# Performance work log

Hardware: AMD Instinct MI355X
Metric: run time of the kernel (lower is better)

The kernel has to match this reference:

```python
import jax, jax.numpy as jnp
import numpy as np

B, Q, K, H, DQ, DK, DV = 16, 128, 512, 128, 128, 128, 128
MASK_VALUE = -1000000.0  # matches d2l.sequence_mask fill value


def setup_inputs() -> dict:
    key = jax.random.key(0)
    ks = jax.random.split(key, 7)
    queries = jax.random.normal(ks[0], (B, Q, DQ), dtype=jnp.float32)
    keys = jax.random.normal(ks[1], (B, K, DK), dtype=jnp.float32)
    values = jax.random.normal(ks[2], (B, K, DV), dtype=jnp.float32)
    valid_lens = jax.random.randint(ks[3], (B,), 1, K + 1, dtype=jnp.int32)
    # Linear params (no bias), scaled like torch default init ~ 1/sqrt(fan_in)
    W_q = jax.random.normal(ks[4], (DQ, H), dtype=jnp.float32) / np.sqrt(DQ)
    W_k = jax.random.normal(ks[5], (DK, H), dtype=jnp.float32) / np.sqrt(DK)
    w_v = jax.random.normal(ks[6], (H,), dtype=jnp.float32) / np.sqrt(H)
    return {"queries": queries, "keys": keys, "values": values,
            "valid_lens": valid_lens, "W_q": W_q, "W_k": W_k, "w_v": w_v}


def reference(queries, keys, values, valid_lens, W_q, W_k, w_v):
    # Project queries and keys: (B,Q,H), (B,K,H)
    q = jnp.einsum("bqd,dh->bqh", queries, W_q)
    k = jnp.einsum("bkd,dh->bkh", keys, W_k)
    # Broadcast add -> tanh -> linear-to-1 score: (B,Q,K)
    features = jnp.tanh(q[:, :, None, :] + k[:, None, :, :])  # (B,Q,K,H)
    scores = jnp.einsum("bqkh,h->bqk", features, w_v)
    # masked softmax over last axis; valid_lens is (B,), broadcast over Q
    mask = jnp.arange(K)[None, None, :] < valid_lens[:, None, None]  # (B,1,K)
    scores = jnp.where(mask, scores, MASK_VALUE)
    attn = jax.nn.softmax(scores, axis=-1)
    # weighted sum over keys: (B,Q,DV)
    return jnp.einsum("bqk,bkv->bqv", attn, values)
```

## Files before the change

### kernel.cpp

```cpp
#include <hip/hip_runtime.h>

#define NB 16
#define NQ 128
#define NK 512
#define NH 128
#define NDV 128

#define KPAD 132

typedef __attribute__((ext_vector_type(8))) short short8;
typedef __attribute__((ext_vector_type(4))) float f32x4;
typedef __attribute__((ext_vector_type(2))) float f32x2;

#define C2LOG2E 2.8853900817779268f
#define LOG2E   1.4426950408889634f

__device__ __forceinline__ short f2bf(float x) {
    unsigned u = __float_as_uint(x);
    unsigned r = (u + 0x7fffu + ((u >> 16) & 1u)) >> 16;
    return (short)r;
}
__device__ __forceinline__ float bf2f(short s) {
    return __uint_as_float(((unsigned)(unsigned short)s) << 16);
}

__global__ __launch_bounds__(256) void wsplit_kernel(
    const float* __restrict__ Wq, const float* __restrict__ Wk,
    const float* __restrict__ wv,
    short* __restrict__ pqh, short* __restrict__ pql,
    short* __restrict__ pkh, short* __restrict__ pkl,
    float* __restrict__ w2)
{
    int blk = blockIdx.x;
    int t   = threadIdx.x;
    if (blk == 0 && t < NH) w2[t] = 2.0f * wv[t];
    int w = blk >> 3, ht = blk & 7;
    int ks = t >> 6, lane = t & 63;
    int m = lane & 15, quad = lane >> 4;
    const float* W = w ? Wk : Wq;
    short* ph = w ? pkh : pqh;
    short* pl = w ? pkl : pql;
    short8 hi, lo;
#pragma unroll
    for (int j = 0; j < 8; ++j) {
        float x = W[(size_t)(ks * 32 + quad * 8 + j) * NH + ht * 16 + m];
        short h = f2bf(x);
        hi[j] = h;
        lo[j] = f2bf(x - bf2f(h));
    }
    size_t o = (size_t)((ht * 4 + ks) * 64 + lane) * 8;
    *(short8*)(ph + o) = hi;
    *(short8*)(pl + o) = lo;
}

__global__ __launch_bounds__(256) void proj_kernel(
    const float* __restrict__ Xq, const float* __restrict__ Xk,
    const short* __restrict__ pqh, const short* __restrict__ pql,
    const short* __restrict__ pkh, const short* __restrict__ pkl,
    float* __restrict__ Eq, float* __restrict__ Ek)
{
    __shared__ float s_x[16 * KPAD];

    int blk = blockIdx.x;
    const float* X; const short* ph; const short* pl; float* Y; int row0;
    if (blk < 128) { X = Xq; ph = pqh; pl = pql; Y = Eq; row0 = blk * 16; }
    else           { X = Xk; ph = pkh; pl = pkl; Y = Ek; row0 = (blk - 128) * 16; }
    int t = threadIdx.x;
    int wave = t >> 6, lane = t & 63;
    int m = lane & 15, quad = lane >> 4;

#pragma unroll
    for (int r = 0; r < 2; ++r) {
        int i = (t + r * 256) * 4;
        int row = i >> 7, col = i & 127;
        *(f32x4*)&s_x[row * KPAD + col] =
            *(const f32x4*)&X[(size_t)(row0 + row) * NH + col];
    }
    __syncthreads();

    short8 AH[4], AL[4];
#pragma unroll
    for (int ks = 0; ks < 4; ++ks) {
        int base = m * KPAD + ks * 32 + quad * 8;
        f32x4 x0 = *(const f32x4*)&s_x[base];
        f32x4 x1 = *(const f32x4*)&s_x[base + 4];
#pragma unroll
        for (int j = 0; j < 4; ++j) {
            short h0 = f2bf(x0[j]);
            AH[ks][j] = h0; AL[ks][j] = f2bf(x0[j] - bf2f(h0));
            short h1 = f2bf(x1[j]);
            AH[ks][j + 4] = h1; AL[ks][j + 4] = f2bf(x1[j] - bf2f(h1));
        }
    }
#pragma unroll
    for (int hi = 0; hi < 2; ++hi) {
        int ht = wave * 2 + hi;
        f32x4 acc = {0.f, 0.f, 0.f, 0.f};
#pragma unroll
        for (int ks = 0; ks < 4; ++ks) {
            size_t o = (size_t)((ht * 4 + ks) * 64 + lane) * 8;
            short8 bh = *(const short8*)(ph + o);
            short8 bl = *(const short8*)(pl + o);
            acc = __builtin_amdgcn_mfma_f32_16x16x32_bf16(AH[ks], bl, acc, 0, 0, 0);
            acc = __builtin_amdgcn_mfma_f32_16x16x32_bf16(AL[ks], bh, acc, 0, 0, 0);
            acc = __builtin_amdgcn_mfma_f32_16x16x32_bf16(AH[ks], bh, acc, 0, 0, 0);
        }
#pragma unroll
        for (int r = 0; r < 4; ++r)
            Y[(size_t)(row0 + quad * 4 + r) * NH + ht * 16 + m] =
                __builtin_amdgcn_exp2f(acc[r] * C2LOG2E);
    }
}

__global__ __launch_bounds__(512) void score_kernel(
    const float* __restrict__ Eqp, const float* __restrict__ Ekp,
    const int* __restrict__ vlen, const float* __restrict__ w2,
    float* __restrict__ P)
{
    __shared__ float s_ek[128 * KPAD];
    __shared__ float s_eq[16 * NH];
    __shared__ float s_w2[NH];

    int blk = blockIdx.x;
    int b    = blk & 15;
    int rest = blk >> 4;
    int qt = rest & 7, kc = rest >> 3;
    int q0 = qt * 16, k0 = kc * 128;
    int t  = threadIdx.x;

    int nv = vlen[b];
    nv = max(1, min(NK, nv));
    float* Pb = P + ((size_t)b * NQ + q0) * NK;

    if (k0 >= nv) {
        int q = t >> 5, kk = (t & 31) * 4;
        f32x4 z = {0.f, 0.f, 0.f, 0.f};
        *(f32x4*)&Pb[(size_t)q * NK + k0 + kk] = z;
        return;
    }

    for (int i = t; i < 128 * 32; i += 512) {
        int row = i >> 5, c4 = i & 31;
        *(f32x4*)&s_ek[row * KPAD + c4 * 4] =
            *(const f32x4*)&Ekp[((size_t)b * NK + k0 + row) * NH + c4 * 4];
    }
    *(f32x4*)&s_eq[t * 4] =
        *(const f32x4*)&Eqp[((size_t)b * NQ + q0) * NH + t * 4];
    if (t < 32) *(f32x4*)&s_w2[t * 4] = *(const f32x4*)&w2[t * 4];
    __syncthreads();

    int lane = t & 63, w = t >> 6;
    int g = w & 3, hf = w >> 2;

    float s2 = s_w2[lane] + s_w2[lane + 64];
#pragma unroll
    for (int off = 32; off; off >>= 1) s2 += __shfl_xor(s2, off);
    float wsum = 0.5f * s2;

    const float* ek = &s_ek[(hf * 64 + lane) * KPAD];
    const float* e0 = &s_eq[(g * 4 + 0) * NH];
    const float* e1 = &s_eq[(g * 4 + 1) * NH];
    const float* e2 = &s_eq[(g * 4 + 2) * NH];
    const float* e3 = &s_eq[(g * 4 + 3) * NH];

    float c00 = 0.f, c01 = 0.f, c10 = 0.f, c11 = 0.f;
    float c20 = 0.f, c21 = 0.f, c30 = 0.f, c31 = 0.f;
#pragma unroll
    for (int hh = 0; hh < NH; hh += 8) {
        f32x4 kA = *(const f32x4*)(ek + hh);
        f32x4 kB = *(const f32x4*)(ek + hh + 4);
        f32x4 wA = *(const f32x4*)(s_w2 + hh);
        f32x4 wB = *(const f32x4*)(s_w2 + hh + 4);
        f32x4 qA0 = *(const f32x4*)(e0 + hh), qB0 = *(const f32x4*)(e0 + hh + 4);
        f32x4 qA1 = *(const f32x4*)(e1 + hh), qB1 = *(const f32x4*)(e1 + hh + 4);
        f32x4 qA2 = *(const f32x4*)(e2 + hh), qB2 = *(const f32x4*)(e2 + hh + 4);
        f32x4 qA3 = *(const f32x4*)(e3 + hh), qB3 = *(const f32x4*)(e3 + hh + 4);
#pragma unroll
        for (int i = 0; i < 4; ++i) {
            c00 = fmaf(wA[i], __builtin_amdgcn_rcpf(fmaf(qA0[i], kA[i], 1.0f)), c00);
            c10 = fmaf(wA[i], __builtin_amdgcn_rcpf(fmaf(qA1[i], kA[i], 1.0f)), c10);
            c20 = fmaf(wA[i], __builtin_amdgcn_rcpf(fmaf(qA2[i], kA[i], 1.0f)), c20);
            c30 = fmaf(wA[i], __builtin_amdgcn_rcpf(fmaf(qA3[i], kA[i], 1.0f)), c30);
            c01 = fmaf(wB[i], __builtin_amdgcn_rcpf(fmaf(qB0[i], kB[i], 1.0f)), c01);
            c11 = fmaf(wB[i], __builtin_amdgcn_rcpf(fmaf(qB1[i], kB[i], 1.0f)), c11);
            c21 = fmaf(wB[i], __builtin_amdgcn_rcpf(fmaf(qB2[i], kB[i], 1.0f)), c21);
            c31 = fmaf(wB[i], __builtin_amdgcn_rcpf(fmaf(qB3[i], kB[i], 1.0f)), c31);
        }
    }
    int kg = k0 + hf * 64 + lane;
    bool valid = kg < nv;
    float p0 = valid ? __builtin_amdgcn_exp2f((wsum - (c00 + c01)) * LOG2E) : 0.f;
    float p1 = valid ? __builtin_amdgcn_exp2f((wsum - (c10 + c11)) * LOG2E) : 0.f;
    float p2 = valid ? __builtin_amdgcn_exp2f((wsum - (c20 + c21)) * LOG2E) : 0.f;
    float p3 = valid ? __builtin_amdgcn_exp2f((wsum - (c30 + c31)) * LOG2E) : 0.f;
    float* Pr = Pb + (size_t)(g * 4) * NK + kg;
    Pr[0 * NK] = p0;
    Pr[1 * NK] = p1;
    Pr[2 * NK] = p2;
    Pr[3 * NK] = p3;
}

__global__ __launch_bounds__(256) void av_kernel(
    const float* __restrict__ P, const float* __restrict__ V,
    const int* __restrict__ vlen, float* __restrict__ out)
{
    __shared__ float s_p[8 * NK];

    int blk = blockIdx.x;
    int b = blk & 15, qt = blk >> 4;
    int q0 = qt * 8;
    int t = threadIdx.x;

    int nv = vlen[b];
    nv = max(1, min(NK, nv));
    int nv8 = (nv + 7) & ~7;

    const f32x4* Pv = (const f32x4*)(P + ((size_t)b * NQ + q0) * NK);
#pragma unroll
    for (int r = 0; r < 4; ++r)
        ((f32x4*)s_p)[t + r * 256] = Pv[t + r * 256];
    __syncthreads();

    int lane = t & 63, w = t >> 6;
    int qa = w * 2, qb = qa + 1;
    const float* pa = &s_p[qa * NK];
    const float* pb = &s_p[qb * NK];

    f32x4 sa0 = *(const f32x4*)(pa + lane * 8);
    f32x4 sa1 = *(const f32x4*)(pa + lane * 8 + 4);
    f32x4 sb0 = *(const f32x4*)(pb + lane * 8);
    f32x4 sb1 = *(const f32x4*)(pb + lane * 8 + 4);
    float sa = ((sa0[0] + sa0[1]) + (sa0[2] + sa0[3])) +
               ((sa1[0] + sa1[1]) + (sa1[2] + sa1[3]));
    float sb = ((sb0[0] + sb0[1]) + (sb0[2] + sb0[3])) +
               ((sb1[0] + sb1[1]) + (sb1[2] + sb1[3]));
#pragma unroll
    for (int off = 32; off; off >>= 1) {
        sa += __shfl_xor(sa, off);
        sb += __shfl_xor(sb, off);
    }
    float ra = 1.0f / sa, rb = 1.0f / sb;

    int dv0 = lane * 2;
    const float* Vb = V + (size_t)b * NK * NDV + dv0;
    float a0 = 0.f, a1 = 0.f, b0 = 0.f, b1 = 0.f;
    for (int k = 0; k < nv8; k += 8) {
        f32x4 PA0 = *(const f32x4*)(pa + k);
        f32x4 PA1 = *(const f32x4*)(pa + k + 4);
        f32x4 PB0 = *(const f32x4*)(pb + k);
        f32x4 PB1 = *(const f32x4*)(pb + k + 4);
        f32x2 v0 = *(const f32x2*)(Vb + (size_t)(k + 0) * NDV);
        f32x2 v1 = *(const f32x2*)(Vb + (size_t)(k + 1) * NDV);
        f32x2 v2 = *(const f32x2*)(Vb + (size_t)(k + 2) * NDV);
        f32x2 v3 = *(const f32x2*)(Vb + (size_t)(k + 3) * NDV);
        f32x2 v4 = *(const f32x2*)(Vb + (size_t)(k + 4) * NDV);
        f32x2 v5 = *(const f32x2*)(Vb + (size_t)(k + 5) * NDV);
        f32x2 v6 = *(const f32x2*)(Vb + (size_t)(k + 6) * NDV);
        f32x2 v7 = *(const f32x2*)(Vb + (size_t)(k + 7) * NDV);
        a0 = fmaf(PA0[0], v0[0], a0); a1 = fmaf(PA0[0], v0[1], a1);
        b0 = fmaf(PB0[0], v0[0], b0); b1 = fmaf(PB0[0], v0[1], b1);
        a0 = fmaf(PA0[1], v1[0], a0); a1 = fmaf(PA0[1], v1[1], a1);
        b0 = fmaf(PB0[1], v1[0], b0); b1 = fmaf(PB0[1], v1[1], b1);
        a0 = fmaf(PA0[2], v2[0], a0); a1 = fmaf(PA0[2], v2[1], a1);
        b0 = fmaf(PB0[2], v2[0], b0); b1 = fmaf(PB0[2], v2[1], b1);
        a0 = fmaf(PA0[3], v3[0], a0); a1 = fmaf(PA0[3], v3[1], a1);
        b0 = fmaf(PB0[3], v3[0], b0); b1 = fmaf(PB0[3], v3[1], b1);
        a0 = fmaf(PA1[0], v4[0], a0); a1 = fmaf(PA1[0], v4[1], a1);
        b0 = fmaf(PB1[0], v4[0], b0); b1 = fmaf(PB1[0], v4[1], b1);
        a0 = fmaf(PA1[1], v5[0], a0); a1 = fmaf(PA1[1], v5[1], a1);
        b0 = fmaf(PB1[1], v5[0], b0); b1 = fmaf(PB1[1], v5[1], b1);
        a0 = fmaf(PA1[2], v6[0], a0); a1 = fmaf(PA1[2], v6[1], a1);
        b0 = fmaf(PB1[2], v6[0], b0); b1 = fmaf(PB1[2], v6[1], b1);
        a0 = fmaf(PA1[3], v7[0], a0); a1 = fmaf(PA1[3], v7[1], a1);
        b0 = fmaf(PB1[3], v7[0], b0); b1 = fmaf(PB1[3], v7[1], b1);
    }
    size_t oa = ((size_t)b * NQ + q0 + qa) * NDV + dv0;
    size_t ob = ((size_t)b * NQ + q0 + qb) * NDV + dv0;
    f32x2 Oa = {a0 * ra, a1 * ra};
    f32x2 Ob = {b0 * rb, b1 * rb};
    *(f32x2*)&out[oa] = Oa;
    *(f32x2*)&out[ob] = Ob;
}

extern "C" void kernel_launch(void* const* d_in, const int* in_sizes, int n_in,
                              void* d_out, int out_size, void* d_ws, size_t ws_size,
                              hipStream_t stream) {
    const float* q  = (const float*)d_in[0];
    const float* ks = (const float*)d_in[1];
    const float* vs = (const float*)d_in[2];
    const int*   vl = (const int*)d_in[3];
    const float* wq = (const float*)d_in[4];
    const float* wk = (const float*)d_in[5];
    const float* wv = (const float*)d_in[6];

    float* Eq = (float*)d_ws;
    float* Ek = Eq + 2048 * 128;
    float* P  = Ek + (size_t)8192 * 128;
    float* w2 = P + (size_t)NB * NQ * NK;
    short* pqh = (short*)(w2 + 128);
    short* pql = pqh + 16384;
    short* pkh = pql + 16384;
    short* pkl = pkh + 16384;

    wsplit_kernel<<<16, 256, 0, stream>>>(wq, wk, wv, pqh, pql, pkh, pkl, w2);
    proj_kernel<<<640, 256, 0, stream>>>(q, ks, pqh, pql, pkh, pkl, Eq, Ek);
    score_kernel<<<512, 512, 0, stream>>>(Eq, Ek, vl, w2, P);
    av_kernel<<<256, 256, 0, stream>>>(P, vs, vl, (float*)d_out);
}
```

Before: 107.9 us.

## Pair reciprocals in score loop, rotate batch mapping, split AV blocks finer

The score kernel now computes two reciprocals with one rcp, using 1/(x1*x2) times the other factor. This trades a transcendental for extra multiplies, and the product could overflow or lose precision. Both score and AV kernels rotate the batch index with the block index so that uneven valid lengths spread across CUs. The AV kernel handles 4 queries per block instead of 8, doubling the grid to 512 blocks for better occupancy and load balance, at the cost of reading V twice as often.

```diff
diff --git a/kernel.cpp b/kernel.cpp
--- a/kernel.cpp
+++ b/kernel.cpp
@@ -122,8 +122,8 @@
     __shared__ float s_w2[NH];
 
     int blk = blockIdx.x;
-    int b    = blk & 15;
-    int rest = blk >> 4;
+    int b    = ((blk & 15) + (blk >> 8)) & 15;
+    int rest = (blk >> 4) & 31;
     int qt = rest & 7, kc = rest >> 3;
     int q0 = qt * 16, k0 = kc * 128;
     int t  = threadIdx.x;
@@ -165,6 +165,16 @@
 
     float c00 = 0.f, c01 = 0.f, c10 = 0.f, c11 = 0.f;
     float c20 = 0.f, c21 = 0.f, c30 = 0.f, c31 = 0.f;
+
+#define PAIR(acc0, acc1, qa, ka, wa, qb, kb, wb)                        \
+    {                                                                   \
+        float x1 = fmaf(qa, ka, 1.0f);                                  \
+        float x2 = fmaf(qb, kb, 1.0f);                                  \
+        float R = __builtin_amdgcn_rcpf(x1 * x2);                       \
+        acc0 = fmaf(wa, R * x2, acc0);                                  \
+        acc1 = fmaf(wb, R * x1, acc1);                                  \
+    }
+
 #pragma unroll
     for (int hh = 0; hh < NH; hh += 8) {
         f32x4 kA = *(const f32x4*)(ek + hh);
@@ -177,16 +187,13 @@
         f32x4 qA3 = *(const f32x4*)(e3 + hh), qB3 = *(const f32x4*)(e3 + hh + 4);
 #pragma unroll
         for (int i = 0; i < 4; ++i) {
-            c00 = fmaf(wA[i], __builtin_amdgcn_rcpf(fmaf(qA0[i], kA[i], 1.0f)), c00);
-            c10 = fmaf(wA[i], __builtin_amdgcn_rcpf(fmaf(qA1[i], kA[i], 1.0f)), c10);
-            c20 = fmaf(wA[i], __builtin_amdgcn_rcpf(fmaf(qA2[i], kA[i], 1.0f)), c20);
-            c30 = fmaf(wA[i], __builtin_amdgcn_rcpf(fmaf(qA3[i], kA[i], 1.0f)), c30);
-            c01 = fmaf(wB[i], __builtin_amdgcn_rcpf(fmaf(qB0[i], kB[i], 1.0f)), c01);
-            c11 = fmaf(wB[i], __builtin_amdgcn_rcpf(fmaf(qB1[i], kB[i], 1.0f)), c11);
-            c21 = fmaf(wB[i], __builtin_amdgcn_rcpf(fmaf(qB2[i], kB[i], 1.0f)), c21);
-            c31 = fmaf(wB[i], __builtin_amdgcn_rcpf(fmaf(qB3[i], kB[i], 1.0f)), c31);
+            PAIR(c00, c01, qA0[i], kA[i], wA[i], qB0[i], kB[i], wB[i]);
+            PAIR(c10, c11, qA1[i], kA[i], wA[i], qB1[i], kB[i], wB[i]);
+            PAIR(c20, c21, qA2[i], kA[i], wA[i], qB2[i], kB[i], wB[i]);
+            PAIR(c30, c31, qA3[i], kA[i], wA[i], qB3[i], kB[i], wB[i]);
         }
     }
+#undef PAIR
     int kg = k0 + hf * 64 + lane;
     bool valid = kg < nv;
     float p0 = valid ? __builtin_amdgcn_exp2f((wsum - (c00 + c01)) * LOG2E) : 0.f;
@@ -204,11 +211,12 @@
     const float* __restrict__ P, const float* __restrict__ V,
     const int* __restrict__ vlen, float* __restrict__ out)
 {
-    __shared__ float s_p[8 * NK];
-
-    int blk = blockIdx.x;
-    int b = blk & 15, qt = blk >> 4;
-    int q0 = qt * 8;
+    __shared__ float s_p[4 * NK];
+
+    int blk = blockIdx.x;
+    int b  = ((blk & 15) + (blk >> 8)) & 15;
+    int qt = (blk >> 4) & 31;
+    int q0 = qt * 4;
     int t = threadIdx.x;
 
     int nv = vlen[b];
@@ -216,39 +224,27 @@
     int nv8 = (nv + 7) & ~7;
 
     const f32x4* Pv = (const f32x4*)(P + ((size_t)b * NQ + q0) * NK);
-#pragma unroll
-    for (int r = 0; r < 4; ++r)
-        ((f32x4*)s_p)[t + r * 256] = Pv[t + r * 256];
+    ((f32x4*)s_p)[t]       = Pv[t];
+    ((f32x4*)s_p)[t + 256] = Pv[t + 256];
     __syncthreads();
 
     int lane = t & 63, w = t >> 6;
-    int qa = w * 2, qb = qa + 1;
-    const float* pa = &s_p[qa * NK];
-    const float* pb = &s_p[qb * NK];
-
-    f32x4 sa0 = *(const f32x4*)(pa + lane * 8);
-    f32x4 sa1 = *(const f32x4*)(pa + lane * 8 + 4);
-    f32x4 sb0 = *(const f32x4*)(pb + lane * 8);
-    f32x4 sb1 = *(const f32x4*)(pb + lane * 8 + 4);
-    float sa = ((sa0[0] + sa0[1]) + (sa0[2] + sa0[3])) +
-               ((sa1[0] + sa1[1]) + (sa1[2] + sa1[3]));
-    float sb = ((sb0[0] + sb0[1]) + (sb0[2] + sb0[3])) +
-               ((sb1[0] + sb1[1]) + (sb1[2] + sb1[3]));
-#pragma unroll
-    for (int off = 32; off; off >>= 1) {
-        sa += __shfl_xor(sa, off);
-        sb += __shfl_xor(sb, off);
-    }
-    float ra = 1.0f / sa, rb = 1.0f / sb;
+    const float* pr = &s_p[w * NK];
+
+    f32x4 s0 = *(const f32x4*)(pr + lane * 8);
+    f32x4 s1 = *(const f32x4*)(pr + lane * 8 + 4);
+    float sm = ((s0[0] + s0[1]) + (s0[2] + s0[3])) +
+               ((s1[0] + s1[1]) + (s1[2] + s1[3]));
+#pragma unroll
+    for (int off = 32; off; off >>= 1) sm += __shfl_xor(sm, off);
+    float rinv = 1.0f / sm;
 
     int dv0 = lane * 2;
     const float* Vb = V + (size_t)b * NK * NDV + dv0;
-    float a0 = 0.f, a1 = 0.f, b0 = 0.f, b1 = 0.f;
+    float o0 = 0.f, o1 = 0.f;
     for (int k = 0; k < nv8; k += 8) {
-        f32x4 PA0 = *(const f32x4*)(pa + k);
-        f32x4 PA1 = *(const f32x4*)(pa + k + 4);
-        f32x4 PB0 = *(const f32x4*)(pb + k);
-        f32x4 PB1 = *(const f32x4*)(pb + k + 4);
+        f32x4 pA = *(const f32x4*)(pr + k);
+        f32x4 pB = *(const f32x4*)(pr + k + 4);
         f32x2 v0 = *(const f32x2*)(Vb + (size_t)(k + 0) * NDV);
         f32x2 v1 = *(const f32x2*)(Vb + (size_t)(k + 1) * NDV);
         f32x2 v2 = *(const f32x2*)(Vb + (size_t)(k + 2) * NDV);
@@ -257,29 +253,18 @@
         f32x2 v5 = *(const f32x2*)(Vb + (size_t)(k + 5) * NDV);
         f32x2 v6 = *(const f32x2*)(Vb + (size_t)(k + 6) * NDV);
         f32x2 v7 = *(const f32x2*)(Vb + (size_t)(k + 7) * NDV);
-        a0 = fmaf(PA0[0], v0[0], a0); a1 = fmaf(PA0[0], v0[1], a1);
-        b0 = fmaf(PB0[0], v0[0], b0); b1 = fmaf(PB0[0], v0[1], b1);
-        a0 = fmaf(PA0[1], v1[0], a0); a1 = fmaf(PA0[1], v1[1], a1);
-        b0 = fmaf(PB0[1], v1[0], b0); b1 = fmaf(PB0[1], v1[1], b1);
-        a0 = fmaf(PA0[2], v2[0], a0); a1 = fmaf(PA0[2], v2[1], a1);
-        b0 = fmaf(PB0[2], v2[0], b0); b1 = fmaf(PB0[2], v2[1], b1);
-        a0 = fmaf(PA0[3], v3[0], a0); a1 = fmaf(PA0[3], v3[1], a1);
-        b0 = fmaf(PB0[3], v3[0], b0); b1 = fmaf(PB0[3], v3[1], b1);
-        a0 = fmaf(PA1[0], v4[0], a0); a1 = fmaf(PA1[0], v4[1], a1);
-        b0 = fmaf(PB1[0], v4[0], b0); b1 = fmaf(PB1[0], v4[1], b1);
-        a0 = fmaf(PA1[1], v5[0], a0); a1 = fmaf(PA1[1], v5[1], a1);
-        b0 = fmaf(PB1[1], v5[0], b0); b1 = fmaf(PB1[1], v5[1], b1);
-        a0 = fmaf(PA1[2], v6[0], a0); a1 = fmaf(PA1[2], v6[1], a1);
-        b0 = fmaf(PB1[2], v6[0], b0); b1 = fmaf(PB1[2], v6[1], b1);
-        a0 = fmaf(PA1[3], v7[0], a0); a1 = fmaf(PA1[3], v7[1], a1);
-        b0 = fmaf(PB1[3], v7[0], b0); b1 = fmaf(PB1[3], v7[1], b1);
-    }
-    size_t oa = ((size_t)b * NQ + q0 + qa) * NDV + dv0;
-    size_t ob = ((size_t)b * NQ + q0 + qb) * NDV + dv0;
-    f32x2 Oa = {a0 * ra, a1 * ra};
-    f32x2 Ob = {b0 * rb, b1 * rb};
-    *(f32x2*)&out[oa] = Oa;
-    *(f32x2*)&out[ob] = Ob;
+        o0 = fmaf(pA[0], v0[0], o0); o1 = fmaf(pA[0], v0[1], o1);
+        o0 = fmaf(pA[1], v1[0], o0); o1 = fmaf(pA[1], v1[1], o1);
+        o0 = fmaf(pA[2], v2[0], o0); o1 = fmaf(pA[2], v2[1], o1);
+        o0 = fmaf(pA[3], v3[0], o0); o1 = fmaf(pA[3], v3[1], o1);
+        o0 = fmaf(pB[0], v4[0], o0); o1 = fmaf(pB[0], v4[1], o1);
+        o0 = fmaf(pB[1], v5[0], o0); o1 = fmaf(pB[1], v5[1], o1);
+        o0 = fmaf(pB[2], v6[0], o0); o1 = fmaf(pB[2], v6[1], o1);
+        o0 = fmaf(pB[3], v7[0], o0); o1 = fmaf(pB[3], v7[1], o1);
+    }
+    size_t ob = ((size_t)b * NQ + q0 + w) * NDV + dv0;
+    f32x2 o = {o0 * rinv, o1 * rinv};
+    *(f32x2*)&out[ob] = o;
 }
 
 extern "C" void kernel_launch(void* const* d_in, const int* in_sizes, int n_in,
@@ -305,5 +290,5 @@
     wsplit_kernel<<<16, 256, 0, stream>>>(wq, wk, wv, pqh, pql, pkh, pkl, w2);
     proj_kernel<<<640, 256, 0, stream>>>(q, ks, pqh, pql, pkh, pkl, Eq, Ek);
     score_kernel<<<512, 512, 0, stream>>>(Eq, Ek, vl, w2, P);
-    av_kernel<<<256, 256, 0, stream>>>(P, vs, vl, (float*)d_out);
-}
+    av_kernel<<<512, 256, 0, stream>>>(P, vs, vl, (float*)d_out);
+}
```

After: 117.3 us. 1.09x slower.
